# Kernel tuning notes

Hardware: AMD Instinct MI355X
Metric: run time of the kernel (lower is better)

Reference implementation:

```python
import jax, jax.numpy as jnp
import numpy as np

NUM_WIRES = 14
N_LAYERS = 3


def setup_inputs() -> dict:
    key = jax.random.key(0)
    k1, k2, k3, k4, k5 = jax.random.split(key, 5)
    B, D = 1024, 2 ** NUM_WIRES
    sr = jax.random.normal(k1, (B, D), dtype=jnp.float32)
    si = jax.random.normal(k2, (B, D), dtype=jnp.float32)
    # normalize each complex state vector (StatePreparation requires unit norm)
    norm = jnp.sqrt(jnp.sum(sr * sr + si * si, axis=-1, keepdims=True))
    sr, si = sr / norm, si / norm
    var_params = jax.random.normal(k3, (N_LAYERS, NUM_WIRES, 3), dtype=jnp.float32)
    head_w = jax.random.normal(k4, (1, NUM_WIRES), dtype=jnp.float32) / np.sqrt(NUM_WIRES)
    head_b = jax.random.normal(k5, (1,), dtype=jnp.float32) * 0.01
    return {"state_real": sr, "state_imag": si, "var_params": var_params,
            "head_w": head_w, "head_b": head_b}


def _apply_1q(psi, U, w):
    # psi: (B, 2, 2, ..., 2); wire w lives on axis 1+w (wire 0 = MSB, PennyLane order)
    psi = jnp.moveaxis(psi, 1 + w, -1)
    psi = jnp.einsum('ij,...j->...i', U, psi)
    return jnp.moveaxis(psi, -1, 1 + w)


def _apply_cnot(psi, c, t):
    psi = jnp.moveaxis(psi, (1 + c, 1 + t), (-2, -1))
    psi = jnp.stack([psi[..., 0, :], psi[..., 1, ::-1]], axis=-2)
    return jnp.moveaxis(psi, (-2, -1), (1 + c, 1 + t))


def _rot_matrix(theta_x, theta_y, theta_z):
    # combined RZ @ RY @ RX (RX applied first), complex64 2x2
    cx, sx = jnp.cos(theta_x / 2), jnp.sin(theta_x / 2)
    cy, sy = jnp.cos(theta_y / 2), jnp.sin(theta_y / 2)
    RX = jnp.array([[cx, -1j * sx], [-1j * sx, cx]], dtype=jnp.complex64)
    RY = jnp.array([[cy, -sy], [sy, cy]], dtype=jnp.complex64)
    ez = jnp.exp(-1j * theta_z.astype(jnp.complex64) / 2)
    RZ = jnp.array([[1.0, 0.0], [0.0, 0.0]], dtype=jnp.complex64) * ez + \
         jnp.array([[0.0, 0.0], [0.0, 1.0]], dtype=jnp.complex64) * jnp.conj(ez)
    return RZ @ RY @ RX


def reference(state_real, state_imag, var_params, head_w, head_b):
    B = state_real.shape[0]
    n = NUM_WIRES
    psi = (state_real + 1j * state_imag).astype(jnp.complex64)
    psi = psi.reshape((B,) + (2,) * n)
    for l in range(N_LAYERS):
        for w in range(n):
            U = _rot_matrix(var_params[l, w, 0], var_params[l, w, 1], var_params[l, w, 2])
            psi = _apply_1q(psi, U, w)
        for w in range(n - 1):
            psi = _apply_cnot(psi, w, w + 1)
        psi = _apply_cnot(psi, n - 1, 0)
    probs = jnp.real(psi * jnp.conj(psi))  # (B, 2, ..., 2)
    feats = []
    all_axes = tuple(range(1, n + 1))
    for w in range(n):
        other = tuple(a for a in all_axes if a != 1 + w)
        m = jnp.sum(probs, axis=other)  # (B, 2)
        feats.append(m[:, 0] - m[:, 1])  # <Z_w>
    features = jnp.stack(feats, axis=-1).astype(jnp.float32)  # (B, num_wires)
    out = features @ head_w.T + head_b  # (B, 1)
    return out.squeeze(-1)
```

## Files before the change

kernel.cpp:

```cpp
#include <hip/hip_runtime.h>

#define NW 14
#define NL 3
#define NGAT 42
#define DIM 16384
#define BLOCK 1024


typedef float        f4  __attribute__((ext_vector_type(4)));
typedef _Float16     h8  __attribute__((ext_vector_type(8)));
typedef unsigned int u4v __attribute__((ext_vector_type(4)));

constexpr int parity14(int v) { int p = 0; for (int i = 0; i < NW; ++i) p ^= (v >> i) & 1; return p; }
constexpr int hibit(int v) { int h = -1; for (int i = 0; i < NW; ++i) if ((v >> i) & 1) h = i; return h; }

struct Lin { int col[NW]; };

constexpr int lin_apply(const Lin& M, int x) {
    int r = 0;
    for (int i = 0; i < NW; ++i) if ((x >> i) & 1) r ^= M.col[i];
    return r;
}
constexpr Lin lin_inverse(const Lin& M) {
    int E[NW] = {}, P[NW] = {};
    for (int i = 0; i < NW; ++i) {
        int v = M.col[i], p = 1 << i;
        while (v) {
            int h = hibit(v);
            if (!E[h]) { E[h] = v; P[h] = p; break; }
            v ^= E[h]; p ^= P[h];
        }
    }
    Lin R{};
    for (int i = 0; i < NW; ++i) {
        int v = 1 << i, p = 0;
        while (v) { int h = hibit(v); v ^= E[h]; p ^= P[h]; }
        R.col[i] = p;
    }
    return R;
}
constexpr Lin lin_compose(const Lin& A, const Lin& B) {
    Lin R{};
    for (int i = 0; i < NW; ++i) R.col[i] = lin_apply(A, B.col[i]);
    return R;
}

struct Alg {
    int ngates[12];
    int gidx[12][4];
    int basisA[12][4];
    int comboA[12][16];
    int cvecA[12][10];
    Lin F[12];
    int Rf[NW];
};

constexpr Alg make_alg() {
    Alg A{};
    int R[NW] = {}, C[NW] = {};
    for (int p = 0; p < NW; ++p) { R[p] = 1 << p; C[p] = 1 << p; }
    int bi = 0;
    for (int l = 0; l < NL; ++l) {
        const int sizes[4] = {4, 4, 4, 2};
        int w0 = 0;
        for (int s = 0; s < 4; ++s) {
            const int ng = sizes[s];
            A.ngates[bi] = ng;
            int basis[4] = {}, rr[4] = {};
            for (int j = 0; j < ng; ++j) {
                int w = w0 + j, p = 13 - w;
                basis[j] = C[p];
                rr[j] = R[p];
                A.gidx[bi][j] = l * NW + w;
            }
            int ech[4] = {}; int ne = 0;
            for (int j = 0; j < ng; ++j) {
                int v = basis[j];
                bool ch = true;
                while (ch) { ch = false;
                    for (int k = 0; k < ne; ++k)
                        if (v && ((v >> hibit(ech[k])) & 1)) { v ^= ech[k]; ch = true; }
                }
                ech[ne++] = v;
            }
            int nb = ng;
            for (int cand = 1; cand < DIM && nb < 4; ++cand) {
                bool ok = true;
                for (int j = 0; j < ng; ++j) if (parity14(cand & rr[j])) { ok = false; break; }
                if (!ok) continue;
                int v = cand;
                bool ch = true;
                while (ch) { ch = false;
                    for (int k = 0; k < ne; ++k)
                        if (v && ((v >> hibit(ech[k])) & 1)) { v ^= ech[k]; ch = true; }
                }
                if (v) { basis[nb++] = cand; ech[ne++] = v; }
            }
            int piv[4] = {};
            for (int k = 0; k < 4; ++k) piv[k] = hibit(ech[k]);
            for (int a = 0; a < 4; ++a)
                for (int b2 = a + 1; b2 < 4; ++b2)
                    if (piv[b2] < piv[a]) { int t = piv[a]; piv[a] = piv[b2]; piv[b2] = t; }
            int npp[10] = {}; int nn = 0;
            for (int bit = 0; bit < NW; ++bit) {
                bool isp = false;
                for (int k = 0; k < 4; ++k) if (piv[k] == bit) isp = true;
                if (!isp) npp[nn++] = bit;
            }
            for (int k = 0; k < 10; ++k) {
                int c = 1 << npp[k];
                for (int j = 0; j < ng; ++j) if ((rr[j] >> npp[k]) & 1) c ^= basis[j];
                A.cvecA[bi][k] = c;
            }
            for (int e = 0; e < 16; ++e) {
                int v = 0;
                for (int j = 0; j < 4; ++j) if ((e >> j) & 1) v ^= basis[j];
                A.comboA[bi][e] = v;
            }
            for (int j = 0; j < 4; ++j) A.basisA[bi][j] = basis[j];
            for (int j = 0; j < 4; ++j) A.F[bi].col[j] = basis[j];
            for (int k = 0; k < 10; ++k) A.F[bi].col[4 + k] = A.cvecA[bi][k];
            w0 += ng;
            ++bi;
        }
        for (int w = 0; w < NW; ++w) {
            int c = w, t = (w + 1) % NW;
            int pc = 13 - c, pt = 13 - t;
            R[pt] ^= R[pc];
            C[pc] ^= C[pt];
        }
    }
    for (int p = 0; p < NW; ++p) A.Rf[p] = R[p];
    return A;
}

constexpr Lin make_fin() {
    Lin F{};
    for (int j = 0; j < 4; ++j) F.col[j]     = 1 << (13 - j);
    for (int j = 0; j < 4; ++j) F.col[4 + j] = 1 << (9 - j);
    for (int k = 0; k < 6; ++k) F.col[8 + k] = 1 << (5 - k);
    return F;
}
constexpr Lin make_fp0() {
    Lin F{};
    for (int j = 0; j < 4; ++j) F.col[j]     = 1 << (9 - j);
    for (int j = 0; j < 4; ++j) F.col[4 + j] = 1 << (13 - j);
    for (int k = 0; k < 6; ++k) F.col[8 + k] = 1 << (5 - k);
    return F;
}
constexpr Lin FIN = make_fin();
constexpr Lin FP0 = make_fp0();

struct Twist { unsigned t[10]; };

constexpr int rankv(const int* v, int nv, int width) {
    int basis[8] = {};
    int rk = 0;
    for (int i = 0; i < nv; ++i) {
        int x = v[i] & ((1 << width) - 1);
        for (int b = width - 1; b >= 0; --b) {
            if (!((x >> b) & 1)) continue;
            if (basis[b]) { x ^= basis[b]; continue; }
            basis[b] = x; ++rk; break;
        }
    }
    return rk;
}

constexpr int img5(int u, const unsigned* t) {
    int r = u & 31;
    for (int k = 0; k < 10; ++k) if ((u >> (4 + k)) & 1) r ^= (int)t[k];
    return r;
}

constexpr int eval5(const unsigned* t, const int (*preR)[5], const int* preS) {
    {
        int w[4] = { 4 ^ (int)((t[0] >> 2) & 7), (int)((t[1] >> 2) & 7),
                     (int)((t[2] >> 2) & 7), (int)((t[3] >> 2) & 7) };
        if (rankv(w, 4, 3) < 3) return -1;
    }
    int sc = 0;
    for (int r = 2; r < 12; ++r) {
        int v[5];
        for (int i = 0; i < 5; ++i) v[i] = img5(preR[r][i], t);
        sc += rankv(v, 5, 5);
    }
    {
        int v[5];
        for (int i = 0; i < 5; ++i) v[i] = img5(preS[i], t);
        sc += rankv(v, 5, 5);
    }
    return sc;
}

constexpr Twist find_twist() {
    Alg A = make_alg();
    int preR[12][5] = {};
    for (int r = 2; r < 12; ++r) {
        Lin Fprev = (r == 2) ? FP0 : A.F[r - 1];
        Lin Fi = lin_inverse(Fprev);
        for (int k = 0; k < 4; ++k) preR[r][k] = lin_apply(Fi, A.cvecA[r][k]);
        preR[r][4] = lin_apply(Fi, A.basisA[r][2]);
    }
    int preS[5] = {};
    {
        Lin F0i = lin_inverse(FIN);
        for (int k = 0; k < 5; ++k) preS[k] = lin_apply(F0i, 1 << (k + 2));
    }
    Twist best{};
    for (int k = 0; k < 10; ++k) best.t[k] = 0;
    int bs = eval5(best.t, preR, preS);
    unsigned x = 0x9E3779B9u;
    for (int s = 0; s < 2; ++s) {
        Twist cur{};
        if (s == 0) {
            for (int k = 0; k < 10; ++k) cur.t[k] = 0;
        } else {
            for (int k = 0; k < 10; ++k) {
                x = x * 1664525u + 1013904223u;
                const unsigned m = (k == 0) ? 3u : 7u;
                cur.t[k] = ((x >> 13) & m) << 2;
            }
        }
        int cs = eval5(cur.t, preR, preS);
        for (int pass = 0; pass < 2; ++pass) {
            for (int k = 0; k < 10; ++k) {
                unsigned bc = cur.t[k];
                int bv = cs;
                const unsigned lim = (k == 0) ? 16u : 32u;
                for (unsigned c = 0; c < lim; c += 4) {
                    cur.t[k] = c;
                    const int e = eval5(cur.t, preR, preS);
                    if (e > bv) { bv = e; bc = c; }
                }
                cur.t[k] = bc;
                cs = bv;
            }
        }
        if (cs > bs) { bs = cs; best = cur; }
    }
    return best;
}

constexpr Twist TW = find_twist();

struct BatchP {
    int ngates;
    int gidx[4];
    unsigned rdy[10];
    unsigned rde[16];
};
struct PlanP {
    BatchP b[12];
    unsigned stB[14];
    unsigned ykey[14];
    int zsel[14];
    unsigned tw[10];
};

constexpr PlanP make_planp() {
    Alg A = make_alg();
    PlanP P{};
    for (int bi = 0; bi < 12; ++bi) {
        P.b[bi].ngates = A.ngates[bi];
        for (int j = 0; j < 4; ++j) P.b[bi].gidx[j] = A.gidx[bi][j];
    }
    Lin T{};
    for (int j = 0; j < 4; ++j) T.col[j] = 1 << j;
    for (int k = 0; k < 10; ++k) T.col[4 + k] = (1 << (4 + k)) ^ (int)TW.t[k];

    {
        Lin L0 = lin_compose(T, lin_inverse(FIN));
        for (int bit = 0; bit < NW; ++bit) P.stB[bit] = (unsigned)lin_apply(L0, 1 << bit) * 4u;
    }
    for (int r = 2; r < 12; ++r) {
        Lin Fprev = (r == 2) ? FP0 : A.F[r - 1];
        Lin Lw = lin_compose(T, lin_inverse(Fprev));
        for (int k = 0; k < 10; ++k) P.b[r].rdy[k] = (unsigned)lin_apply(Lw, A.cvecA[r][k]) * 4u;
        for (int e = 0; e < 16; ++e) P.b[r].rde[e] = (unsigned)lin_apply(Lw, A.comboA[r][e]) * 4u;
    }
    for (int w = 0; w < NW; ++w) {
        int zrw = A.Rf[13 - w];
        unsigned ym = 0;
        for (int k = 0; k < 10; ++k) ym |= (unsigned)parity14(A.cvecA[11][k] & zrw) << k;
        int qm = parity14(A.basisA[11][2] & zrw) | (parity14(A.basisA[11][3] & zrw) << 1);
        P.ykey[w] = ym | ((unsigned)qm << 10);
        P.zsel[w] = parity14(A.basisA[11][0] & zrw) | (parity14(A.basisA[11][1] & zrw) << 1);
    }
    for (int k = 0; k < 10; ++k) P.tw[k] = TW.t[k];
    return P;
}

constexpr PlanP PL = make_planp();

constexpr unsigned TILE_OFF[4] = {
    0u,
    (1u << 10) ^ (PL.tw[4] << 2),
    (1u << 11) ^ (PL.tw[5] << 2),
    (1u << 10) ^ (1u << 11) ^ ((PL.tw[4] ^ PL.tw[5]) << 2)
};

__device__ __forceinline__ unsigned pk_rn(float r, float i) {
    const unsigned hr = (unsigned)__builtin_bit_cast(unsigned short, (_Float16)r);
    const unsigned hi = (unsigned)__builtin_bit_cast(unsigned short, (_Float16)i);
    return hr | (hi << 16);
}
__device__ __forceinline__ float2 up(unsigned d) {
    float2 c;
    c.x = (float)__builtin_bit_cast(_Float16, (unsigned short)(d & 0xffffu));
    c.y = (float)__builtin_bit_cast(_Float16, (unsigned short)(d >> 16));
    return c;
}

__device__ __forceinline__ f4 mfh(u4v a, u4v b, f4 c) {
    return __builtin_amdgcn_mfma_f32_16x16x32_f16(
        __builtin_bit_cast(h8, a), __builtin_bit_cast(h8, b), c, 0, 0, 0);
}

#define RD_SREP(B)                                                     \
    unsigned srep = 0;                                                 \
    srep ^= (n & 1u)   ? B.rdy[0] : 0u;                                \
    srep ^= (n & 2u)   ? B.rdy[1] : 0u;                                \
    srep ^= (n & 4u)   ? B.rdy[2] : 0u;                                \
    srep ^= (n & 8u)   ? B.rdy[3] : 0u;                                \
    srep ^= (wid & 1u) ? B.rdy[6] : 0u;                                \
    srep ^= (wid & 2u) ? B.rdy[7] : 0u;                                \
    srep ^= (wid & 4u) ? B.rdy[8] : 0u;                                \
    srep ^= (wid & 8u) ? B.rdy[9] : 0u;                                \
    srep ^= (q & 1u)   ? B.rde[4] : 0u;                                \
    srep ^= (q & 2u)   ? B.rde[8] : 0u;

__device__ __forceinline__ void mfma_pair0(char* __restrict__ lds, const float* __restrict__ gm,
                                           unsigned* __restrict__ atab, const unsigned bnq) {
    const unsigned tid = threadIdx.x;
    const unsigned lane = tid & 63u, wid = tid >> 6;
    const unsigned n = lane & 15u, q = lane >> 4;

    __syncthreads();

    if (tid < 512) {
        const unsigned idx = tid & 255u;
        const unsigned m = idx >> 4, ein = idx & 15u;
        const int gbase = (tid < 256) ? 0 : 4;
        float wr = 1.f, wi = 0.f;
        #pragma unroll
        for (int j = 0; j < 4; ++j) {
            const unsigned mj = (m >> j) & 1u, ej = (ein >> j) & 1u;
            const float ur = gm[(gbase + j) * 8 + (int)(mj * 4u + ej * 2u)];
            const float ui = gm[(gbase + j) * 8 + (int)(mj * 4u + ej * 2u) + 1];
            const float nr = wr * ur - wi * ui;
            const float ni = wr * ui + wi * ur;
            wr = nr; wi = ni;
        }
        const unsigned o = m * 16u + (ein ^ (m & 12u));
        unsigned* __restrict__ tab = atab + ((tid < 256) ? 0 : 512);
        tab[o]        = pk_rn(wr, -wi);
        tab[256 + o]  = pk_rn(wi, wr);
    }

    u4v bfr[4];
    #pragma unroll
    for (int t = 0; t < 4; ++t) {
        bfr[t] = *(const u4v*)(lds + (bnq ^ TILE_OFF[t]));
    }

    __syncthreads();

    const unsigned tix = (n << 4) + (((q << 2) ^ (n & 12u)));
    const u4v War = *(const u4v*)&atab[tix];
    const u4v Wai = *(const u4v*)&atab[256 + tix];
    const u4v Wbr = *(const u4v*)&atab[512 + tix];
    const u4v Wbi = *(const u4v*)&atab[768 + tix];

    #pragma unroll
    for (int t = 0; t < 4; ++t) {
        f4 dr = {0.f, 0.f, 0.f, 0.f};
        f4 di = {0.f, 0.f, 0.f, 0.f};
        dr = mfh(bfr[t], War, dr);
        di = mfh(bfr[t], Wai, di);
        u4v pb;
        pb.x = pk_rn(dr.x, di.x);
        pb.y = pk_rn(dr.y, di.y);
        pb.z = pk_rn(dr.z, di.z);
        pb.w = pk_rn(dr.w, di.w);
        f4 ar = {0.f, 0.f, 0.f, 0.f};
        f4 ai = {0.f, 0.f, 0.f, 0.f};
        ar = mfh(Wbr, pb, ar);
        ai = mfh(Wbi, pb, ai);
        u4v s;
        s.x = pk_rn(ar.x, ai.x);
        s.y = pk_rn(ar.y, ai.y);
        s.z = pk_rn(ar.z, ai.z);
        s.w = pk_rn(ar.w, ai.w);
        *(u4v*)(lds + (bnq ^ TILE_OFF[t])) = s;
    }
}

template <int BI>
__device__ __forceinline__ void mfma_batch(char* __restrict__ lds, const float* __restrict__ gm,
                                           unsigned* __restrict__ atab, const unsigned bnq) {
    constexpr BatchP B = PL.b[BI];
    const unsigned tid = threadIdx.x;
    const unsigned lane = tid & 63u, wid = tid >> 6;
    const unsigned n = lane & 15u, q = lane >> 4;

    __syncthreads();

    if (tid < 256) {
        const unsigned m = tid >> 4, ein = tid & 15u;
        float wr = 1.f, wi = 0.f;
        #pragma unroll
        for (int j = 0; j < 4; ++j) {
            if (j < B.ngates) {
                const unsigned mj = (m >> j) & 1u, ej = (ein >> j) & 1u;
                const float ur = gm[B.gidx[j] * 8 + (int)(mj * 4u + ej * 2u)];
                const float ui = gm[B.gidx[j] * 8 + (int)(mj * 4u + ej * 2u) + 1];
                const float nr = wr * ur - wi * ui;
                const float ni = wr * ui + wi * ur;
                wr = nr; wi = ni;
            }
        }
        if (B.ngates < 4 && (((m ^ ein) >> B.ngates) != 0u)) { wr = 0.f; wi = 0.f; }
        const unsigned o = m * 16u + (ein ^ (m & 12u));
        atab[o]        = pk_rn(wr, -wi);
        atab[256 + o]  = pk_rn(wi, wr);
    }

    u4v bfr[4];
    {
        RD_SREP(B)
        #pragma unroll
        for (int t = 0; t < 4; ++t) {
            const unsigned st = srep ^ ((t & 1) ? B.rdy[4] : 0u) ^ ((t & 2) ? B.rdy[5] : 0u);
            const unsigned c0 = *(const unsigned*)(lds + st);
            const unsigned c1 = *(const unsigned*)(lds + (st ^ B.rde[1]));
            const unsigned c2 = *(const unsigned*)(lds + (st ^ B.rde[2]));
            const unsigned c3 = *(const unsigned*)(lds + (st ^ B.rde[3]));
            u4v v; v.x = c0; v.y = c1; v.z = c2; v.w = c3;
            bfr[t] = v;
        }
    }

    __syncthreads();

    const unsigned tix = (n << 4) + (((q << 2) ^ (n & 12u)));
    const u4v A0 = *(const u4v*)&atab[tix];
    const u4v A1 = *(const u4v*)&atab[256 + tix];

    #pragma unroll
    for (int t = 0; t < 4; ++t) {
        f4 ar = {0.f, 0.f, 0.f, 0.f};
        f4 ai = {0.f, 0.f, 0.f, 0.f};
        ar = mfh(A0, bfr[t], ar);
        ai = mfh(A1, bfr[t], ai);
        u4v s;
        s.x = pk_rn(ar.x, ai.x);
        s.y = pk_rn(ar.y, ai.y);
        s.z = pk_rn(ar.z, ai.z);
        s.w = pk_rn(ar.w, ai.w);
        *(u4v*)(lds + (bnq ^ TILE_OFF[t])) = s;
    }
}

#define BFC(A, B_, ua, ub) { const float2 t0 = A, t1 = B_; \
    A.x  = ua.x * t0.x - ua.y * t0.y + ua.z * t1.x - ua.w * t1.y; \
    A.y  = ua.x * t0.y + ua.y * t0.x + ua.z * t1.y + ua.w * t1.x; \
    B_.x = ub.x * t0.x - ub.y * t0.y + ub.z * t1.x - ub.w * t1.y; \
    B_.y = ub.x * t0.y + ub.y * t0.x + ub.z * t1.y + ub.w * t1.x; }

__device__ __forceinline__ float tail_batch(char* __restrict__ lds, const float* __restrict__ gm,
                                            const float* __restrict__ g_hw) {
    constexpr BatchP B = PL.b[11];
    const unsigned tid = threadIdx.x;
    const unsigned lane = tid & 63u, wid = tid >> 6;
    const unsigned n = lane & 15u, q = lane >> 4;
    __syncthreads();
    const f4 u0a = *(const f4*)&gm[B.gidx[0] * 8];
    const f4 u0b = *(const f4*)&gm[B.gidx[0] * 8 + 4];
    const f4 u1a = *(const f4*)&gm[B.gidx[1] * 8];
    const f4 u1b = *(const f4*)&gm[B.gidx[1] * 8 + 4];
    float hwv[NW];
    #pragma unroll
    for (int w = 0; w < NW; ++w) hwv[w] = g_hw[w];
    float acc = 0.f;
    RD_SREP(B)
    #pragma unroll
    for (int t = 0; t < 4; ++t) {
        const unsigned st = srep ^ ((t & 1) ? B.rdy[4] : 0u) ^ ((t & 2) ? B.rdy[5] : 0u);
        float2 c0 = up(*(const unsigned*)(lds + st));
        float2 c1 = up(*(const unsigned*)(lds + (st ^ B.rde[1])));
        float2 c2 = up(*(const unsigned*)(lds + (st ^ B.rde[2])));
        float2 c3 = up(*(const unsigned*)(lds + (st ^ B.rde[3])));
        BFC(c0, c1, u0a, u0b)  BFC(c2, c3, u0a, u0b)
        BFC(c0, c2, u1a, u1b)  BFC(c1, c3, u1a, u1b)
        const float p0 = c0.x * c0.x + c0.y * c0.y;
        const float p1 = c1.x * c1.x + c1.y * c1.y;
        const float p2 = c2.x * c2.x + c2.y * c2.y;
        const float p3 = c3.x * c3.x + c3.y * c3.y;
        const float sa = p0 + p1, sb = p0 - p1, sc = p2 + p3, sd = p2 - p3;
        const float W4[4] = {sa + sc, sb + sd, sa - sc, sb - sd};
        const unsigned y = (wid << 6) | ((unsigned)t << 4) | n;
        const unsigned key = y | (q << 10);
        #pragma unroll
        for (int w = 0; w < NW; ++w) {
            const unsigned sg = ((unsigned)__popc(key & PL.ykey[w])) << 31;
            const float s = __uint_as_float(__float_as_uint(hwv[w]) ^ sg);
            acc += W4[PL.zsel[w]] * s;
        }
    }
    return acc;
}

__global__ __launch_bounds__(BLOCK, 8) void qsim_kernel(
    const float* __restrict__ g_sr, const float* __restrict__ g_si,
    const float* __restrict__ g_params, const float* __restrict__ g_hw,
    const float* __restrict__ g_hb, float* __restrict__ g_out)
{
    extern __shared__ char lds[];
    __shared__ __align__(16) float gm[NGAT * 8];
    __shared__ __align__(16) unsigned atab[1024];
    __shared__ float red[BLOCK / 64];

    const unsigned tid = threadIdx.x;
    const int b = blockIdx.x;
    const float* __restrict__ srcr = g_sr + (size_t)b * DIM;
    const float* __restrict__ srci = g_si + (size_t)b * DIM;

    if (tid < NGAT) {
        const float tx = g_params[tid * 3 + 0];
        const float ty = g_params[tid * 3 + 1];
        const float tz = g_params[tid * 3 + 2];
        const float cx = cosf(0.5f * tx), sx = sinf(0.5f * tx);
        const float cy = cosf(0.5f * ty), sy = sinf(0.5f * ty);
        const float cz = cosf(0.5f * tz), sz = sinf(0.5f * tz);
        const float a00r = cy * cx,  a00i = sy * sx;
        const float a01r = -sy * cx, a01i = -cy * sx;
        const float a10r = sy * cx,  a10i = -cy * sx;
        const float a11r = cy * cx,  a11i = -sy * sx;
        gm[tid * 8 + 0] = cz * a00r + sz * a00i;
        gm[tid * 8 + 1] = cz * a00i - sz * a00r;
        gm[tid * 8 + 2] = cz * a01r + sz * a01i;
        gm[tid * 8 + 3] = cz * a01i - sz * a01r;
        gm[tid * 8 + 4] = cz * a10r - sz * a10i;
        gm[tid * 8 + 5] = cz * a10i + sz * a10r;
        gm[tid * 8 + 6] = cz * a11r - sz * a11i;
        gm[tid * 8 + 7] = cz * a11i + sz * a11r;
    }

    const unsigned lane0 = tid & 63u, wid0 = tid >> 6;
    const unsigned n0 = lane0 & 15u, q0 = lane0 >> 4;
    unsigned twv = 0;
    #pragma unroll
    for (int k = 0; k < 4; ++k) twv ^= ((n0 >> k) & 1u) ? PL.tw[k] : 0u;
    #pragma unroll
    for (int k = 0; k < 4; ++k) twv ^= ((wid0 >> k) & 1u) ? PL.tw[6 + k] : 0u;
    const unsigned bnq = ((wid0 << 10) ^ (n0 << 4) ^ (q0 << 2) ^ twv) << 2;

    unsigned bb = 0;
    #pragma unroll
    for (int k = 0; k < 10; ++k) bb ^= ((tid >> k) & 1u) ? PL.stB[k + 2] : 0u;
    #pragma unroll
    for (int it = 0; it < 4; ++it) {
        const int x = (int)tid * 4 + it * 4096;
        const f4 r4 = *(const f4*)(srcr + x);
        const f4 i4 = *(const f4*)(srci + x);
        const unsigned base = bb ^ ((it & 1) ? PL.stB[12] : 0u) ^ ((it & 2) ? PL.stB[13] : 0u);
        *(unsigned*)(lds + base) = pk_rn(r4.x, i4.x);
        *(unsigned*)(lds + (base ^ PL.stB[0])) = pk_rn(r4.y, i4.y);
        *(unsigned*)(lds + (base ^ PL.stB[1])) = pk_rn(r4.z, i4.z);
        *(unsigned*)(lds + (base ^ (PL.stB[0] ^ PL.stB[1]))) = pk_rn(r4.w, i4.w);
    }

    mfma_pair0(lds, gm, atab, bnq);
    mfma_batch<2>(lds, gm, atab, bnq);
    mfma_batch<3>(lds, gm, atab, bnq);
    mfma_batch<4>(lds, gm, atab, bnq);
    mfma_batch<5>(lds, gm, atab, bnq);
    mfma_batch<6>(lds, gm, atab, bnq);
    mfma_batch<7>(lds, gm, atab, bnq);
    mfma_batch<8>(lds, gm, atab, bnq);
    mfma_batch<9>(lds, gm, atab, bnq);
    mfma_batch<10>(lds, gm, atab, bnq);

    float acc = tail_batch(lds, gm, g_hw);

    #pragma unroll
    for (int off = 32; off > 0; off >>= 1) acc += __shfl_down(acc, off);
    const int lane = tid & 63, wid = tid >> 6;
    if (lane == 0) red[wid] = acc;
    __syncthreads();
    if (tid == 0) {
        float s = 0.0f;
        #pragma unroll
        for (int k = 0; k < BLOCK / 64; ++k) s += red[k];
        g_out[b] = s + g_hb[0];
    }
}

extern "C" void kernel_launch(void* const* d_in, const int* in_sizes, int n_in,
                              void* d_out, int out_size, void* d_ws, size_t ws_size,
                              hipStream_t stream) {
    const float* sr = (const float*)d_in[0];
    const float* si = (const float*)d_in[1];
    const float* vp = (const float*)d_in[2];
    const float* hw = (const float*)d_in[3];
    const float* hb = (const float*)d_in[4];
    float* out = (float*)d_out;

    dim3 grid(out_size);
    dim3 block(BLOCK);
    size_t shmem = (size_t)DIM * 4;
    qsim_kernel<<<grid, block, shmem, stream>>>(sr, si, vp, hw, hb, out);
}
```

Before: 186.8 us.

## Fuse layer-1 gate batches four and five into a paired MFMA pass

Replaces two separate mfma_batch passes (batches 4 and 5, the first eight rotations of layer 1) with a single mfma_pair2 pass. It applies two chained 16x16 MFMA gate products per tile, like mfma_pair0, and derives a new compile-time linear basis-change plan so the LDS addressing and the twist search stay consistent. This removes one full LDS read/write sweep and a pair of barriers per state vector. In exchange it adds an extra fp16 rounding step within the fused pair and more complex constexpr planning.

```diff
diff --git a/kernel.cpp b/kernel.cpp
--- a/kernel.cpp
+++ b/kernel.cpp
@@ -151,6 +151,64 @@
 constexpr Lin FIN = make_fin();
 constexpr Lin FP0 = make_fp0();
 
+struct PairAlg {
+    int gA[4]; int gB[4];
+    int bA[4]; int bB[4];
+    int pyd[6];
+    Lin Fout;
+};
+
+constexpr PairAlg make_pair_l1() {
+    int R[NW] = {}, C[NW] = {};
+    for (int p = 0; p < NW; ++p) { R[p] = 1 << p; C[p] = 1 << p; }
+    for (int w = 0; w < NW; ++w) {
+        int c = w, t = (w + 1) % NW;
+        int pc = 13 - c, pt = 13 - t;
+        R[pt] ^= R[pc];
+        C[pc] ^= C[pt];
+    }
+    PairAlg P{};
+    int rA[4] = {}, rB[4] = {};
+    for (int j = 0; j < 4; ++j) {
+        int p = 13 - j;
+        P.bA[j] = C[p]; rA[j] = R[p];
+        P.gA[j] = 1 * NW + j;
+    }
+    for (int j = 0; j < 4; ++j) {
+        int p = 13 - (4 + j);
+        P.bB[j] = C[p]; rB[j] = R[p];
+        P.gB[j] = 1 * NW + 4 + j;
+    }
+    int ech[8] = {}; int ne = 0;
+    for (int s = 0; s < 8; ++s) {
+        int v = (s < 4) ? P.bA[s] : P.bB[s - 4];
+        bool ch = true;
+        while (ch) { ch = false;
+            for (int k = 0; k < ne; ++k)
+                if (v && ((v >> hibit(ech[k])) & 1)) { v ^= ech[k]; ch = true; }
+        }
+        ech[ne++] = v;
+    }
+    int piv[8] = {};
+    for (int k = 0; k < 8; ++k) piv[k] = hibit(ech[k]);
+    int nn = 0;
+    for (int bit = 0; bit < NW && nn < 6; ++bit) {
+        bool isp = false;
+        for (int k = 0; k < 8; ++k) if (piv[k] == bit) isp = true;
+        if (!isp) {
+            int u = 1 << bit, d = u;
+            for (int j = 0; j < 4; ++j) if (parity14(rA[j] & u)) d ^= P.bA[j];
+            for (int j = 0; j < 4; ++j) if (parity14(rB[j] & u)) d ^= P.bB[j];
+            P.pyd[nn++] = d;
+        }
+    }
+    for (int j = 0; j < 4; ++j) P.Fout.col[j]     = P.bB[j];
+    for (int j = 0; j < 4; ++j) P.Fout.col[4 + j] = P.bA[j];
+    for (int k = 0; k < 6; ++k) P.Fout.col[8 + k] = P.pyd[k];
+    return P;
+}
+constexpr PairAlg P2A = make_pair_l1();
+
 struct Twist { unsigned t[10]; };
 
 constexpr int rankv(const int* v, int nv, int width) {
@@ -180,7 +238,7 @@
         if (rankv(w, 4, 3) < 3) return -1;
     }
     int sc = 0;
-    for (int r = 2; r < 12; ++r) {
+    for (int r = 0; r < 10; ++r) {
         int v[5];
         for (int i = 0; i < 5; ++i) v[i] = img5(preR[r][i], t);
         sc += rankv(v, 5, 5);
@@ -195,12 +253,32 @@
 
 constexpr Twist find_twist() {
     Alg A = make_alg();
-    int preR[12][5] = {};
-    for (int r = 2; r < 12; ++r) {
-        Lin Fprev = (r == 2) ? FP0 : A.F[r - 1];
-        Lin Fi = lin_inverse(Fprev);
-        for (int k = 0; k < 4; ++k) preR[r][k] = lin_apply(Fi, A.cvecA[r][k]);
-        preR[r][4] = lin_apply(Fi, A.basisA[r][2]);
+    int preR[10][5] = {};
+    int idx = 0;
+    {
+        Lin Fi = lin_inverse(FP0);
+        for (int k = 0; k < 4; ++k) preR[idx][k] = lin_apply(Fi, A.cvecA[2][k]);
+        preR[idx][4] = lin_apply(Fi, A.basisA[2][2]); ++idx;
+    }
+    {
+        Lin Fi = lin_inverse(A.F[2]);
+        for (int k = 0; k < 4; ++k) preR[idx][k] = lin_apply(Fi, A.cvecA[3][k]);
+        preR[idx][4] = lin_apply(Fi, A.basisA[3][2]); ++idx;
+    }
+    {
+        Lin Fi = lin_inverse(A.F[3]);
+        for (int k = 0; k < 4; ++k) preR[idx][k] = lin_apply(Fi, P2A.bB[k]);
+        preR[idx][4] = lin_apply(Fi, P2A.bA[2]); ++idx;
+    }
+    {
+        Lin Fi = lin_inverse(P2A.Fout);
+        for (int k = 0; k < 4; ++k) preR[idx][k] = lin_apply(Fi, A.cvecA[6][k]);
+        preR[idx][4] = lin_apply(Fi, A.basisA[6][2]); ++idx;
+    }
+    for (int r = 7; r < 12; ++r) {
+        Lin Fi = lin_inverse(A.F[r - 1]);
+        for (int k = 0; k < 4; ++k) preR[idx][k] = lin_apply(Fi, A.cvecA[r][k]);
+        preR[idx][4] = lin_apply(Fi, A.basisA[r][2]); ++idx;
     }
     int preS[5] = {};
     {
@@ -250,8 +328,14 @@
     unsigned rdy[10];
     unsigned rde[16];
 };
+struct Pair2P {
+    int gA[4]; int gB[4];
+    unsigned rdy[10];
+    unsigned rde[16];
+};
 struct PlanP {
     BatchP b[12];
+    Pair2P p2;
     unsigned stB[14];
     unsigned ykey[14];
     int zsel[14];
@@ -274,10 +358,24 @@
         for (int bit = 0; bit < NW; ++bit) P.stB[bit] = (unsigned)lin_apply(L0, 1 << bit) * 4u;
     }
     for (int r = 2; r < 12; ++r) {
-        Lin Fprev = (r == 2) ? FP0 : A.F[r - 1];
+        if (r == 4 || r == 5) continue;
+        Lin Fprev = (r == 2) ? FP0 : (r == 6) ? P2A.Fout : A.F[r - 1];
         Lin Lw = lin_compose(T, lin_inverse(Fprev));
         for (int k = 0; k < 10; ++k) P.b[r].rdy[k] = (unsigned)lin_apply(Lw, A.cvecA[r][k]) * 4u;
         for (int e = 0; e < 16; ++e) P.b[r].rde[e] = (unsigned)lin_apply(Lw, A.comboA[r][e]) * 4u;
+    }
+    {
+        Lin Lw = lin_compose(T, lin_inverse(A.F[3]));
+        for (int j = 0; j < 4; ++j) { P.p2.gA[j] = P2A.gA[j]; P.p2.gB[j] = P2A.gB[j]; }
+        for (int k = 0; k < 4; ++k) P.p2.rdy[k] = (unsigned)lin_apply(Lw, P2A.bB[k]) * 4u;
+        P.p2.rdy[4] = (unsigned)lin_apply(Lw, P2A.pyd[0]) * 4u;
+        P.p2.rdy[5] = (unsigned)lin_apply(Lw, P2A.pyd[1]) * 4u;
+        for (int k = 0; k < 4; ++k) P.p2.rdy[6 + k] = (unsigned)lin_apply(Lw, P2A.pyd[2 + k]) * 4u;
+        for (int e = 0; e < 16; ++e) {
+            int v = 0;
+            for (int j = 0; j < 4; ++j) if ((e >> j) & 1) v ^= P2A.bA[j];
+            P.p2.rde[e] = (unsigned)lin_apply(Lw, v) * 4u;
+        }
     }
     for (int w = 0; w < NW; ++w) {
         int zrw = A.Rf[13 - w];
@@ -333,7 +431,7 @@
 __device__ __forceinline__ void mfma_pair0(char* __restrict__ lds, const float* __restrict__ gm,
                                            unsigned* __restrict__ atab, const unsigned bnq) {
     const unsigned tid = threadIdx.x;
-    const unsigned lane = tid & 63u, wid = tid >> 6;
+    const unsigned lane = tid & 63u;
     const unsigned n = lane & 15u, q = lane >> 4;
 
     __syncthreads();
@@ -362,6 +460,82 @@
     #pragma unroll
     for (int t = 0; t < 4; ++t) {
         bfr[t] = *(const u4v*)(lds + (bnq ^ TILE_OFF[t]));
+    }
+
+    __syncthreads();
+
+    const unsigned tix = (n << 4) + (((q << 2) ^ (n & 12u)));
+    const u4v War = *(const u4v*)&atab[tix];
+    const u4v Wai = *(const u4v*)&atab[256 + tix];
+    const u4v Wbr = *(const u4v*)&atab[512 + tix];
+    const u4v Wbi = *(const u4v*)&atab[768 + tix];
+
+    #pragma unroll
+    for (int t = 0; t < 4; ++t) {
+        f4 dr = {0.f, 0.f, 0.f, 0.f};
+        f4 di = {0.f, 0.f, 0.f, 0.f};
+        dr = mfh(bfr[t], War, dr);
+        di = mfh(bfr[t], Wai, di);
+        u4v pb;
+        pb.x = pk_rn(dr.x, di.x);
+        pb.y = pk_rn(dr.y, di.y);
+        pb.z = pk_rn(dr.z, di.z);
+        pb.w = pk_rn(dr.w, di.w);
+        f4 ar = {0.f, 0.f, 0.f, 0.f};
+        f4 ai = {0.f, 0.f, 0.f, 0.f};
+        ar = mfh(Wbr, pb, ar);
+        ai = mfh(Wbi, pb, ai);
+        u4v s;
+        s.x = pk_rn(ar.x, ai.x);
+        s.y = pk_rn(ar.y, ai.y);
+        s.z = pk_rn(ar.z, ai.z);
+        s.w = pk_rn(ar.w, ai.w);
+        *(u4v*)(lds + (bnq ^ TILE_OFF[t])) = s;
+    }
+}
+
+__device__ __forceinline__ void mfma_pair2(char* __restrict__ lds, const float* __restrict__ gm,
+                                           unsigned* __restrict__ atab, const unsigned bnq) {
+    constexpr Pair2P P = PL.p2;
+    const unsigned tid = threadIdx.x;
+    const unsigned lane = tid & 63u, wid = tid >> 6;
+    const unsigned n = lane & 15u, q = lane >> 4;
+
+    __syncthreads();
+
+    if (tid < 512) {
+        const unsigned idx = tid & 255u;
+        const unsigned m = idx >> 4, ein = idx & 15u;
+        float wr = 1.f, wi = 0.f;
+        #pragma unroll
+        for (int j = 0; j < 4; ++j) {
+            const int gi = (tid < 256) ? P.gA[j] : P.gB[j];
+            const unsigned mj = (m >> j) & 1u, ej = (ein >> j) & 1u;
+            const float ur = gm[gi * 8 + (int)(mj * 4u + ej * 2u)];
+            const float ui = gm[gi * 8 + (int)(mj * 4u + ej * 2u) + 1];
+            const float nr = wr * ur - wi * ui;
+            const float ni = wr * ui + wi * ur;
+            wr = nr; wi = ni;
+        }
+        const unsigned o = m * 16u + (ein ^ (m & 12u));
+        unsigned* __restrict__ tab = atab + ((tid < 256) ? 0 : 512);
+        tab[o]        = pk_rn(wr, -wi);
+        tab[256 + o]  = pk_rn(wi, wr);
+    }
+
+    u4v bfr[4];
+    {
+        RD_SREP(P)
+        #pragma unroll
+        for (int t = 0; t < 4; ++t) {
+            const unsigned st = srep ^ ((t & 1) ? P.rdy[4] : 0u) ^ ((t & 2) ? P.rdy[5] : 0u);
+            const unsigned c0 = *(const unsigned*)(lds + st);
+            const unsigned c1 = *(const unsigned*)(lds + (st ^ P.rde[1]));
+            const unsigned c2 = *(const unsigned*)(lds + (st ^ P.rde[2]));
+            const unsigned c3 = *(const unsigned*)(lds + (st ^ P.rde[3]));
+            u4v v; v.x = c0; v.y = c1; v.z = c2; v.w = c3;
+            bfr[t] = v;
+        }
     }
 
     __syncthreads();
@@ -574,8 +748,7 @@
     mfma_pair0(lds, gm, atab, bnq);
     mfma_batch<2>(lds, gm, atab, bnq);
     mfma_batch<3>(lds, gm, atab, bnq);
-    mfma_batch<4>(lds, gm, atab, bnq);
-    mfma_batch<5>(lds, gm, atab, bnq);
+    mfma_pair2(lds, gm, atab, bnq);
     mfma_batch<6>(lds, gm, atab, bnq);
     mfma_batch<7>(lds, gm, atab, bnq);
     mfma_batch<8>(lds, gm, atab, bnq);
```

After: 188.9 us. Within noise of the previous version (+1.1%).
